# Kernel optimization log

Measured on AMD Instinct MI355X. Metric: run time of the kernel, lower is better.

Reference implementation:

```python
import jax, jax.numpy as jnp
import numpy as np

TMSG = 15  # max_len - 1


def setup_inputs() -> dict:
    key = jax.random.key(0)
    ks = jax.random.split(key, 8)
    B, T_in, E, H, V = 4096, 4, 256, 512, 32000
    s = lambda k, shape: jax.random.normal(k, shape, jnp.float32) * 0.05
    return {
        "inp": jax.random.normal(ks[0], (B, T_in, E), jnp.float32),
        "Wx0": s(ks[1], (E, 4 * H)),
        "Wh0": s(ks[2], (H, 4 * H)),
        "b0": jnp.zeros((4 * H,), jnp.float32),
        "Wx1": s(ks[3], (H, 4 * H)),
        "Wh1": s(ks[4], (H, 4 * H)),
        "b1": jnp.zeros((4 * H,), jnp.float32),
        "Wd": s(ks[5], (H, V)),
        "bd": jnp.zeros((V,), jnp.float32),
    }


def _lstm_step(x, h, c, Wx, Wh, b):
    # Keras LSTMCell gate order: i, f, g(cell), o
    z = x @ Wx + h @ Wh + b
    i, f, g, o = jnp.split(z, 4, axis=-1)
    c = jax.nn.sigmoid(f) * c + jax.nn.sigmoid(i) * jnp.tanh(g)
    h = jax.nn.sigmoid(o) * jnp.tanh(c)
    return h, c


def reference(inp, Wx0, Wh0, b0, Wx1, Wh1, b1, Wd, bd):
    B = inp.shape[0]
    H = Wh0.shape[0]
    z = jnp.zeros((B, H), inp.dtype)

    def scan_fn(carry, x_t):
        h0, c0, h1, c1 = carry
        h0, c0 = _lstm_step(x_t, h0, c0, Wx0, Wh0, b0)
        h1, c1 = _lstm_step(h0, h1, c1, Wx1, Wh1, b1)
        return (h0, c0, h1, c1), None

    # NOTE: source bug resets initial_state to None every step, so each of the
    # max_len-1 steps runs the identical stacked LSTM from zero state; we run it once.
    (h0, c0, h1, c1), _ = jax.lax.scan(scan_fn, (z, z, z, z), jnp.swapaxes(inp, 0, 1))
    out = h1  # (B, H) last-step output of top cell

    log_probs = jax.nn.log_softmax(out @ Wd + bd, axis=-1)  # (B, V)
    probs = jnp.exp(log_probs)
    entropy = -jnp.sum(probs * log_probs, axis=-1)  # (B,)

    keys = jax.random.split(jax.random.key(42), TMSG)
    samples = jax.vmap(lambda k: jax.random.categorical(k, log_probs, axis=-1))(keys)  # (T, B)
    lp = log_probs[jnp.arange(B)[None, :], samples]  # (T, B) log_prob of sampled chars
    ent = jnp.broadcast_to(entropy[None], (TMSG, B))  # (T, B)

    message = samples.T  # (B, T)
    message = jnp.concatenate([message, jnp.zeros_like(message)], axis=1)  # (B, 2T)
    state_h = jnp.stack([h0, c0])  # keras unpack quirk: states[0] = [h, c] of cell 0
    return (message, lp, ent, state_h)
```

## Files before the change

kernel.cpp:

```cpp
#include <hip/hip_runtime.h>
#include <stdint.h>
#include <math.h>

#define BB 4096
#define HH 512
#define VV 32000
#define NT 15
#define STF 2097152

struct KeysArg { uint32_t w[2*NT]; };

__host__ __device__ inline void tf2x32(uint32_t k0, uint32_t k1,
                                       uint32_t x0, uint32_t x1,
                                       uint32_t& o0, uint32_t& o1) {
  uint32_t ks2 = k0 ^ k1 ^ 0x1BD11BDAu;
  x0 += k0; x1 += k1;
#define TF_R(r) { x0 += x1; x1 = (x1 << (r)) | (x1 >> (32 - (r))); x1 ^= x0; }
  TF_R(13) TF_R(15) TF_R(26) TF_R(6)
  x0 += k1; x1 += ks2 + 1u;
  TF_R(17) TF_R(29) TF_R(16) TF_R(24)
  x0 += ks2; x1 += k0 + 2u;
  TF_R(13) TF_R(15) TF_R(26) TF_R(6)
  x0 += k0; x1 += k1 + 3u;
  TF_R(17) TF_R(29) TF_R(16) TF_R(24)
  x0 += k1; x1 += ks2 + 4u;
  TF_R(13) TF_R(15) TF_R(26) TF_R(6)
  x0 += ks2; x1 += k0 + 5u;
#undef TF_R
  o0 = x0; o1 = x1;
}

__global__ __launch_bounds__(256)
void gemm_sk(const float* __restrict__ A0, int lda0,
             const float* __restrict__ W0, int koff0,
             const float* __restrict__ A1, int lda1,
             const float* __restrict__ W1, int koff1,
             int ldw, int Klen,
             const float* __restrict__ bias,
             float* __restrict__ C0, float* __restrict__ C1, int ldc)
{
  const float* A; const float* W; float* C; int lda, koff;
  if (blockIdx.z == 0) { A = A0; lda = lda0; W = W0; koff = koff0; C = C0; }
  else                 { A = A1; lda = lda1; W = W1; koff = koff1; C = C1; }

  __shared__ float As[16][128];
  __shared__ float Ws[16][128];
  const int tid = threadIdx.x;
  const int m0 = blockIdx.y * 128;
  const int n0 = blockIdx.x * 128;
  const int tx = tid & 15, ty = tid >> 4;
  float acc[8][8];
  #pragma unroll
  for (int i = 0; i < 8; ++i)
    #pragma unroll
    for (int j = 0; j < 8; ++j) acc[i][j] = 0.0f;

  const int sr = tid >> 1, sc = (tid & 1) * 8;
  const int wk = tid >> 4, wn = (tid & 15) * 4;

  const int nkt = Klen >> 4;
  for (int kt = 0; kt < nkt; ++kt) {
    const int k0 = koff + (kt << 4);
    const float* asrc = A + (size_t)(m0 + sr) * lda + (k0 + sc);
    float4 av0 = *(const float4*)asrc;
    float4 av1 = *(const float4*)(asrc + 4);
    const float* wsrc = W + (size_t)(k0 + wk) * ldw + (n0 + wn);
    float4 wv0 = *(const float4*)wsrc;
    float4 wv1 = *(const float4*)(wsrc + 64);
    As[sc+0][sr]=av0.x; As[sc+1][sr]=av0.y; As[sc+2][sr]=av0.z; As[sc+3][sr]=av0.w;
    As[sc+4][sr]=av1.x; As[sc+5][sr]=av1.y; As[sc+6][sr]=av1.z; As[sc+7][sr]=av1.w;
    *(float4*)&Ws[wk][wn]      = wv0;
    *(float4*)&Ws[wk][wn + 64] = wv1;
    __syncthreads();
    #pragma unroll
    for (int kk = 0; kk < 16; ++kk) {
      float4 a0 = *(const float4*)&As[kk][ty*8];
      float4 a1 = *(const float4*)&As[kk][ty*8+4];
      float4 b0 = *(const float4*)&Ws[kk][tx*4];
      float4 b1 = *(const float4*)&Ws[kk][tx*4+64];
      float ar[8] = {a0.x,a0.y,a0.z,a0.w,a1.x,a1.y,a1.z,a1.w};
      float br[8] = {b0.x,b0.y,b0.z,b0.w,b1.x,b1.y,b1.z,b1.w};
      #pragma unroll
      for (int i = 0; i < 8; ++i)
        #pragma unroll
        for (int j = 0; j < 8; ++j)
          acc[i][j] = fmaf(ar[i], br[j], acc[i][j]);
    }
    __syncthreads();
  }

  #pragma unroll
  for (int i = 0; i < 8; ++i) {
    const int m = m0 + ty*8 + i;
    float* dst = C + (size_t)m * ldc + (n0 + wn);
    float4 o0, o1;
    o0.x = acc[i][0]; o0.y = acc[i][1]; o0.z = acc[i][2]; o0.w = acc[i][3];
    o1.x = acc[i][4]; o1.y = acc[i][5]; o1.z = acc[i][6]; o1.w = acc[i][7];
    if (bias) {
      o0.x += bias[n0+wn+0]; o0.y += bias[n0+wn+1];
      o0.z += bias[n0+wn+2]; o0.w += bias[n0+wn+3];
      o1.x += bias[n0+wn+64]; o1.y += bias[n0+wn+65];
      o1.z += bias[n0+wn+66]; o1.w += bias[n0+wn+67];
    }
    *(float4*)dst        = o0;
    *(float4*)(dst + 64) = o1;
  }
}

__global__ __launch_bounds__(256)
void gate_kernel(const float* __restrict__ zx, int zxs,
                 const float* __restrict__ z0, const float* __restrict__ z1,
                 const float* __restrict__ bias,
                 const float* __restrict__ cin,
                 float* __restrict__ hout, float* __restrict__ cout,
                 float* __restrict__ sh, float* __restrict__ sc)
{
  int idx = blockIdx.x * 256 + threadIdx.x;
  int b = idx >> 9, j = idx & 511;
  const size_t r2 = (size_t)b * 2048;
  float zi, zf, zg, zo;
  zi = z0[r2+j]      + z1[r2+j]      + bias[j];
  zf = z0[r2+j+512]  + z1[r2+j+512]  + bias[j+512];
  zg = z0[r2+j+1024] + z1[r2+j+1024] + bias[j+1024];
  zo = z0[r2+j+1536] + z1[r2+j+1536] + bias[j+1536];
  if (zx) {
    const size_t rx = (size_t)b * zxs;
    zi += zx[rx+j]; zf += zx[rx+j+512]; zg += zx[rx+j+1024]; zo += zx[rx+j+1536];
  }
  float si = 1.0f/(1.0f+expf(-zi));
  float sf = 1.0f/(1.0f+expf(-zf));
  float so = 1.0f/(1.0f+expf(-zo));
  float c = sf * cin[idx] + si * tanhf(zg);
  float h = so * tanhf(c);
  cout[idx] = c; hout[idx] = h;
  if (sh) { sh[idx] = h; sc[idx] = c; }
}

__global__ __launch_bounds__(256)
void rowstat_kernel(const float* __restrict__ logits,
                    float* __restrict__ rowM, float* __restrict__ rowLS,
                    float* __restrict__ rowEnt)
{
  const int row = blockIdx.x;
  const float* x = logits + (size_t)row * VV;
  const int tid = threadIdx.x;
  float m = -INFINITY;
  for (int v = tid; v < VV; v += 256) m = fmaxf(m, x[v]);
  #pragma unroll
  for (int off = 32; off; off >>= 1) m = fmaxf(m, __shfl_down(m, off));
  __shared__ float sm[4], ssum[4], swsum[4];
  if ((tid & 63) == 0) sm[tid >> 6] = m;
  __syncthreads();
  m = fmaxf(fmaxf(sm[0], sm[1]), fmaxf(sm[2], sm[3]));
  float s = 0.0f, w = 0.0f;
  for (int v = tid; v < VV; v += 256) {
    float d = x[v] - m;
    float e = expf(d);
    s += e; w += d * e;
  }
  #pragma unroll
  for (int off = 32; off; off >>= 1) { s += __shfl_down(s, off); w += __shfl_down(w, off); }
  if ((tid & 63) == 0) { ssum[tid >> 6] = s; swsum[tid >> 6] = w; }
  __syncthreads();
  if (tid == 0) {
    s = ssum[0]+ssum[1]+ssum[2]+ssum[3];
    w = swsum[0]+swsum[1]+swsum[2]+swsum[3];
    float ls = logf(s);
    rowM[row] = m; rowLS[row] = ls; rowEnt[row] = ls - w / s;
  }
}

__global__ __launch_bounds__(256)
void sample_kernel(const float* __restrict__ logits,
                   const float* __restrict__ rowM, const float* __restrict__ rowLS,
                   const float* __restrict__ rowEnt,
                   float* __restrict__ out,
                   KeysArg keys, int bbase)
{
  const int l = blockIdx.x;
  const int b = bbase + l;
  const float* x = logits + (size_t)l * VV;
  const float m = rowM[l], ls = rowLS[l];

  float bv[NT];
  uint32_t bi[NT];
  #pragma unroll
  for (int t = 0; t < NT; ++t) { bv[t] = -INFINITY; bi[t] = 0; }

  const uint32_t pbase = (uint32_t)b * (uint32_t)VV;
  for (int v = threadIdx.x; v < VV; v += 256) {
    const float lp = (x[v] - m) - ls;
    const uint32_t p = pbase + (uint32_t)v;
    #pragma unroll
    for (int t = 0; t < NT; ++t) {
      uint32_t o0, o1;
      tf2x32(keys.w[2*t], keys.w[2*t+1], 0u, p, o0, o1);
      const uint32_t bits = o0 ^ o1;
      float u = fmaxf(__uint_as_float((bits >> 9) | 0x3f800000u) - 1.0f,
                      1.17549435e-38f);
      float g = -logf(-logf(u)) + lp;
      if (g > bv[t]) { bv[t] = g; bi[t] = (uint32_t)v; }
    }
  }

  __shared__ float rv[NT][4];
  __shared__ uint32_t ri[NT][4];
  const int lane = threadIdx.x & 63, wq = threadIdx.x >> 6;
  #pragma unroll
  for (int t = 0; t < NT; ++t) {
    float v = bv[t]; uint32_t idx = bi[t];
    #pragma unroll
    for (int off = 32; off; off >>= 1) {
      float ov = __shfl_down(v, off);
      uint32_t oi = __shfl_down(idx, off);
      if (ov > v || (ov == v && oi < idx)) { v = ov; idx = oi; }
    }
    if (lane == 0) { rv[t][wq] = v; ri[t][wq] = idx; }
  }
  __syncthreads();
  if (threadIdx.x < NT) {
    const int t = threadIdx.x;
    float v = rv[t][0]; uint32_t idx = ri[t][0];
    #pragma unroll
    for (int q = 1; q < 4; ++q) {
      float ov = rv[t][q]; uint32_t oi = ri[t][q];
      if (ov > v || (ov == v && oi < idx)) { v = ov; idx = oi; }
    }
    out[(size_t)b * 30 + t]      = (float)idx;
    out[(size_t)b * 30 + 15 + t] = 0.0f;
    out[122880 + (size_t)t * BB + b] = (x[idx] - m) - ls;
    out[184320 + (size_t)t * BB + b] = rowEnt[l];
  }
}

extern "C" void kernel_launch(void* const* d_in, const int* in_sizes, int n_in,
                              void* d_out, int out_size, void* d_ws, size_t ws_size,
                              hipStream_t stream)
{
  const float* inp = (const float*)d_in[0];
  const float* Wx0 = (const float*)d_in[1];
  const float* Wh0 = (const float*)d_in[2];
  const float* b0v = (const float*)d_in[3];
  const float* Wx1 = (const float*)d_in[4];
  const float* Wh1 = (const float*)d_in[5];
  const float* b1v = (const float*)d_in[6];
  const float* Wd  = (const float*)d_in[7];
  const float* bdv = (const float*)d_in[8];
  float* out = (float*)d_out;
  float* ws = (float*)d_ws;

  float* h0 = ws;
  float* c0 = ws + (size_t)STF;
  float* h1 = ws + (size_t)2*STF;
  float* c1 = ws + (size_t)3*STF;
  float* rowM  = ws + (size_t)4*STF;
  float* rowLS = rowM + 4096;
  float* rowEnt = rowLS + 4096;
  float* logits = ws + (size_t)4*STF + 12288;
  float* zxpre = logits;
  float* z0 = zxpre + (size_t)16384*2048;
  float* z1 = z0 + (size_t)4096*2048;

  size_t ws_floats = ws_size / 4;
  size_t base = (size_t)4*STF + 12288;
  int CH = 4096;
  while (CH > 128 && base + (size_t)CH*VV > ws_floats) CH >>= 1;

  hipMemsetAsync(ws, 0, (size_t)4*STF*sizeof(float), stream);

  gemm_sk<<<dim3(2048/128, 16384/128, 1), 256, 0, stream>>>(
      inp, 256, Wx0, 0,  nullptr, 0, nullptr, 0,
      2048, 256, nullptr, zxpre, nullptr, 2048);

  for (int t = 0; t < 4; ++t) {
    gemm_sk<<<dim3(2048/128, 4096/128, 2), 256, 0, stream>>>(
        h0, 512, Wh0, 0,  h0, 512, Wh0, 256,
        2048, 256, nullptr, z0, z1, 2048);
    gate_kernel<<<STF/256, 256, 0, stream>>>(
        zxpre + t*2048, 8192, z0, z1, b0v, c0, h0, c0,
        (t==3) ? out + 245760 : (float*)nullptr,
        (t==3) ? out + 245760 + STF : (float*)nullptr);
    gemm_sk<<<dim3(2048/128, 4096/128, 2), 256, 0, stream>>>(
        h0, 512, Wx1, 0,  h1, 512, Wh1, 0,
        2048, 512, nullptr, z0, z1, 2048);
    gate_kernel<<<STF/256, 256, 0, stream>>>(
        nullptr, 0, z0, z1, b1v, c1, h1, c1, (float*)nullptr, (float*)nullptr);
  }

  KeysArg ka;
  for (int t = 0; t < NT; ++t) {
    uint32_t o0, o1;
    tf2x32(0u, 42u, 0u, (uint32_t)t, o0, o1);
    ka.w[2*t] = o0; ka.w[2*t+1] = o1;
  }

  const int nch = 4096 / CH;
  for (int c = 0; c < nch; ++c) {
    int bbase = c * CH;
    gemm_sk<<<dim3(VV/128, CH/128, 1), 256, 0, stream>>>(
        h1 + (size_t)bbase*512, 512, Wd, 0,  nullptr, 0, nullptr, 0,
        VV, 512, bdv, logits, nullptr, VV);
    rowstat_kernel<<<CH, 256, 0, stream>>>(logits, rowM, rowLS, rowEnt);
    sample_kernel<<<CH, 256, 0, stream>>>(logits, rowM, rowLS, rowEnt, out, ka, bbase);
  }
}
```

Baseline: 8.274 ms.

## Prune Gumbel sampling with running-max threshold and split samples across blocks

```diff
diff --git a/kernel.cpp b/kernel.cpp
--- a/kernel.cpp
+++ b/kernel.cpp
@@ -32,16 +32,16 @@
 
 __global__ __launch_bounds__(256)
 void gemm_sk(const float* __restrict__ A0, int lda0,
-             const float* __restrict__ W0, int koff0,
+             const float* __restrict__ W0, int koff0, int Klen0,
              const float* __restrict__ A1, int lda1,
-             const float* __restrict__ W1, int koff1,
-             int ldw, int Klen,
+             const float* __restrict__ W1, int koff1, int Klen1,
+             int ldw,
              const float* __restrict__ bias,
              float* __restrict__ C0, float* __restrict__ C1, int ldc)
 {
-  const float* A; const float* W; float* C; int lda, koff;
-  if (blockIdx.z == 0) { A = A0; lda = lda0; W = W0; koff = koff0; C = C0; }
-  else                 { A = A1; lda = lda1; W = W1; koff = koff1; C = C1; }
+  const float* A; const float* W; float* C; int lda, koff, Klen;
+  if (blockIdx.z == 0) { A = A0; lda = lda0; W = W0; koff = koff0; Klen = Klen0; C = C0; }
+  else                 { A = A1; lda = lda1; W = W1; koff = koff1; Klen = Klen1; C = C1; }
 
   __shared__ float As[16][128];
   __shared__ float Ws[16][128];
@@ -108,8 +108,7 @@
 }
 
 __global__ __launch_bounds__(256)
-void gate_kernel(const float* __restrict__ zx, int zxs,
-                 const float* __restrict__ z0, const float* __restrict__ z1,
+void gate_kernel(const float* __restrict__ z0, const float* __restrict__ z1,
                  const float* __restrict__ bias,
                  const float* __restrict__ cin,
                  float* __restrict__ hout, float* __restrict__ cout,
@@ -118,15 +117,10 @@
   int idx = blockIdx.x * 256 + threadIdx.x;
   int b = idx >> 9, j = idx & 511;
   const size_t r2 = (size_t)b * 2048;
-  float zi, zf, zg, zo;
-  zi = z0[r2+j]      + z1[r2+j]      + bias[j];
-  zf = z0[r2+j+512]  + z1[r2+j+512]  + bias[j+512];
-  zg = z0[r2+j+1024] + z1[r2+j+1024] + bias[j+1024];
-  zo = z0[r2+j+1536] + z1[r2+j+1536] + bias[j+1536];
-  if (zx) {
-    const size_t rx = (size_t)b * zxs;
-    zi += zx[rx+j]; zf += zx[rx+j+512]; zg += zx[rx+j+1024]; zo += zx[rx+j+1536];
-  }
+  float zi = z0[r2+j]      + z1[r2+j]      + bias[j];
+  float zf = z0[r2+j+512]  + z1[r2+j+512]  + bias[j+512];
+  float zg = z0[r2+j+1024] + z1[r2+j+1024] + bias[j+1024];
+  float zo = z0[r2+j+1536] + z1[r2+j+1536] + bias[j+1536];
   float si = 1.0f/(1.0f+expf(-zi));
   float sf = 1.0f/(1.0f+expf(-zf));
   float so = 1.0f/(1.0f+expf(-zo));
@@ -177,53 +171,59 @@
                    float* __restrict__ out,
                    KeysArg keys, int bbase)
 {
-  const int l = blockIdx.x;
+  const int l = blockIdx.x / NT;
+  const int t = blockIdx.x % NT;
   const int b = bbase + l;
   const float* x = logits + (size_t)l * VV;
   const float m = rowM[l], ls = rowLS[l];
-
-  float bv[NT];
-  uint32_t bi[NT];
-  #pragma unroll
-  for (int t = 0; t < NT; ++t) { bv[t] = -INFINITY; bi[t] = 0; }
+  const uint32_t k0 = keys.w[2*t], k1 = keys.w[2*t+1];
+
+  float bv = -INFINITY;
+  uint32_t bi = 0;
+  uint32_t thr_ub = 0;
 
   const uint32_t pbase = (uint32_t)b * (uint32_t)VV;
   for (int v = threadIdx.x; v < VV; v += 256) {
-    const float lp = (x[v] - m) - ls;
-    const uint32_t p = pbase + (uint32_t)v;
-    #pragma unroll
-    for (int t = 0; t < NT; ++t) {
-      uint32_t o0, o1;
-      tf2x32(keys.w[2*t], keys.w[2*t+1], 0u, p, o0, o1);
-      const uint32_t bits = o0 ^ o1;
-      float u = fmaxf(__uint_as_float((bits >> 9) | 0x3f800000u) - 1.0f,
-                      1.17549435e-38f);
-      float g = -logf(-logf(u)) + lp;
-      if (g > bv[t]) { bv[t] = g; bi[t] = (uint32_t)v; }
-    }
-  }
-
-  __shared__ float rv[NT][4];
-  __shared__ uint32_t ri[NT][4];
+    uint32_t o0, o1;
+    tf2x32(k0, k1, 0u, pbase + (uint32_t)v, o0, o1);
+    const uint32_t ub = (o0 ^ o1) >> 9;
+    if (__any(ub >= thr_ub)) {
+      float uf = __uint_as_float(ub | 0x3f800000u);
+      float u = fmaxf(uf - 1.0f, 1.17549435e-38f);
+      float g = -logf(-logf(u)) + ((x[v] - m) - ls);
+      bool improved = (ub >= thr_ub) && (g > bv);
+      if (improved) { bv = g; bi = (uint32_t)v; }
+      if (__any(improved)) {
+        float wb = bv;
+        #pragma unroll
+        for (int off = 1; off < 64; off <<= 1)
+          wb = fmaxf(wb, __shfl_xor(wb, off));
+        float us = expf(-expf(-(wb + ls)));
+        float thrf = 1.0f + us * 0.999999f;
+        thr_ub = __float_as_uint(thrf) - 0x3f800000u;
+      }
+    }
+  }
+
+  __shared__ float rv[4];
+  __shared__ uint32_t ri[4];
   const int lane = threadIdx.x & 63, wq = threadIdx.x >> 6;
-  #pragma unroll
-  for (int t = 0; t < NT; ++t) {
-    float v = bv[t]; uint32_t idx = bi[t];
+  {
+    float v = bv; uint32_t idx = bi;
     #pragma unroll
     for (int off = 32; off; off >>= 1) {
       float ov = __shfl_down(v, off);
       uint32_t oi = __shfl_down(idx, off);
       if (ov > v || (ov == v && oi < idx)) { v = ov; idx = oi; }
     }
-    if (lane == 0) { rv[t][wq] = v; ri[t][wq] = idx; }
+    if (lane == 0) { rv[wq] = v; ri[wq] = idx; }
   }
   __syncthreads();
-  if (threadIdx.x < NT) {
-    const int t = threadIdx.x;
-    float v = rv[t][0]; uint32_t idx = ri[t][0];
+  if (threadIdx.x == 0) {
+    float v = rv[0]; uint32_t idx = ri[0];
     #pragma unroll
     for (int q = 1; q < 4; ++q) {
-      float ov = rv[t][q]; uint32_t oi = ri[t][q];
+      float ov = rv[q]; uint32_t oi = ri[q];
       if (ov > v || (ov == v && oi < idx)) { v = ov; idx = oi; }
     }
     out[(size_t)b * 30 + t]      = (float)idx;
@@ -256,10 +256,10 @@
   float* rowM  = ws + (size_t)4*STF;
   float* rowLS = rowM + 4096;
   float* rowEnt = rowLS + 4096;
-  float* logits = ws + (size_t)4*STF + 12288;
-  float* zxpre = logits;
-  float* z0 = zxpre + (size_t)16384*2048;
-  float* z1 = z0 + (size_t)4096*2048;
+  float* region = ws + (size_t)4*STF + 12288;
+  float* z0 = region;
+  float* z1 = region + (size_t)4096*2048;
+  float* logits = region;
 
   size_t ws_floats = ws_size / 4;
   size_t base = (size_t)4*STF + 12288;
@@ -268,23 +268,21 @@
 
   hipMemsetAsync(ws, 0, (size_t)4*STF*sizeof(float), stream);
 
-  gemm_sk<<<dim3(2048/128, 16384/128, 1), 256, 0, stream>>>(
-      inp, 256, Wx0, 0,  nullptr, 0, nullptr, 0,
-      2048, 256, nullptr, zxpre, nullptr, 2048);
-
   for (int t = 0; t < 4; ++t) {
     gemm_sk<<<dim3(2048/128, 4096/128, 2), 256, 0, stream>>>(
-        h0, 512, Wh0, 0,  h0, 512, Wh0, 256,
-        2048, 256, nullptr, z0, z1, 2048);
+        h0, 512, Wh0, 0, 512,
+        inp + t*256, 1024, Wx0, 0, 256,
+        2048, nullptr, z0, z1, 2048);
     gate_kernel<<<STF/256, 256, 0, stream>>>(
-        zxpre + t*2048, 8192, z0, z1, b0v, c0, h0, c0,
+        z0, z1, b0v, c0, h0, c0,
         (t==3) ? out + 245760 : (float*)nullptr,
         (t==3) ? out + 245760 + STF : (float*)nullptr);
     gemm_sk<<<dim3(2048/128, 4096/128, 2), 256, 0, stream>>>(
-        h0, 512, Wx1, 0,  h1, 512, Wh1, 0,
-        2048, 512, nullptr, z0, z1, 2048);
+        h0, 512, Wx1, 0, 512,
+        h1, 512, Wh1, 0, 512,
+        2048, nullptr, z0, z1, 2048);
     gate_kernel<<<STF/256, 256, 0, stream>>>(
-        nullptr, 0, z0, z1, b1v, c1, h1, c1, (float*)nullptr, (float*)nullptr);
+        z0, z1, b1v, c1, h1, c1, (float*)nullptr, (float*)nullptr);
   }
 
   KeysArg ka;
@@ -298,9 +296,10 @@
   for (int c = 0; c < nch; ++c) {
     int bbase = c * CH;
     gemm_sk<<<dim3(VV/128, CH/128, 1), 256, 0, stream>>>(
-        h1 + (size_t)bbase*512, 512, Wd, 0,  nullptr, 0, nullptr, 0,
-        VV, 512, bdv, logits, nullptr, VV);
+        h1 + (size_t)bbase*512, 512, Wd, 0, 512,
+        nullptr, 0, nullptr, 0, 0,
+        VV, bdv, logits, nullptr, VV);
     rowstat_kernel<<<CH, 256, 0, stream>>>(logits, rowM, rowLS, rowEnt);
-    sample_kernel<<<CH, 256, 0, stream>>>(logits, rowM, rowLS, rowEnt, out, ka, bbase);
-  }
-}
+    sample_kernel<<<CH * NT, 256, 0, stream>>>(logits, rowM, rowLS, rowEnt, out, ka, bbase);
+  }
+}
```

After: 8.434 ms. Within noise of the previous version (+1.9%).
